# Kernel tuning notes

Measured on AMD Instinct MI355X. Metric: run time of the kernel, lower is better.

Reference implementation:

```python
import jax, jax.numpy as jnp
import numpy as np

T, B, S, H, E, V = 16, 32, 256, 256, 300, 1000


def setup_inputs() -> dict:
    key = jax.random.key(0)
    ks = jax.random.split(key, 16)
    p = lambda k, shp: (jax.random.normal(k, shp, dtype=jnp.float32) * 0.05)
    return {
        "target_variable": jax.random.randint(ks[0], (T, B), 0, V),
        "h0": p(ks[1], (1, B, H)),
        "c0": p(ks[2], (1, B, H)),
        "encoder_outputs": jax.random.normal(ks[3], (S, B, H), dtype=jnp.float32),
        "encoder_lens": jax.random.randint(ks[4], (B,), 1, S + 1),
        "embedding": p(ks[5], (V, E)),
        "W_ih": p(ks[6], (4 * H, E)),
        "W_hh": p(ks[7], (4 * H, H)),
        "b_ih": p(ks[8], (4 * H,)),
        "b_hh": p(ks[9], (4 * H,)),
        "We": p(ks[10], (H, H)),
        "be": p(ks[11], (H,)),
        "Wd": p(ks[12], (H, H)),
        "bd": p(ks[13], (H,)),
        "wa": p(ks[14], (H,)),
        "ba": p(ks[14], (1,)),
        "W_out": p(ks[15], (V, 2 * H)),
        "b_out": p(ks[15], (V,)),
    }


def _lstm(x, h0, c0, W_ih, W_hh, b_ih, b_hh):
    # x: [T,B,E]; torch gate order i,f,g,o
    x_proj = jnp.einsum('tbe,ge->tbg', x, W_ih) + b_ih  # [T,B,4H]
    def step(carry, xg):
        h, c = carry
        g = xg + h @ W_hh.T + b_hh
        i, f, gg, o = jnp.split(g, 4, axis=-1)
        c = jax.nn.sigmoid(f) * c + jax.nn.sigmoid(i) * jnp.tanh(gg)
        h = jax.nn.sigmoid(o) * jnp.tanh(c)
        return (h, c), h
    (hT, cT), outs = jax.lax.scan(step, (h0[0], c0[0]), x_proj)
    return outs, hT[None], cT[None]


def reference(target_variable, h0, c0, encoder_outputs, encoder_lens,
              embedding, W_ih, W_hh, b_ih, b_hh,
              We, be, Wd, bd, wa, ba, W_out, b_out):
    emb = embedding[target_variable]                      # [T,B,E] (dropout p=0 -> identity)
    output, hT, cT = _lstm(emb, h0, c0, W_ih, W_hh, b_ih, b_hh)  # output [T,B,H]
    # additive attention: same math as expand+Linear, applied before broadcast
    enc_t = jnp.einsum('sbh,gh->sbg', encoder_outputs, We) + be   # [S,B,H]
    dec_t = jnp.einsum('tbh,gh->tbg', output, Wd) + bd            # [T,B,H]
    scores = jnp.einsum('tsbh,h->tsb', jnp.tanh(enc_t[None, :, :, :] + dec_t[:, None, :, :]), wa) + ba[0]
    raw_attention = jnp.transpose(scores, (2, 0, 1))              # [B,T,S]
    valid = (jnp.arange(S)[None, None, :] < encoder_lens[:, None, None])  # [B,1,S]
    raw_attention = jnp.where(valid, raw_attention, -jnp.inf)
    attention = jax.nn.softmax(raw_attention, axis=2)             # [B,T,S]
    enc_bf = jnp.transpose(encoder_outputs, (1, 0, 2))            # [B,S,H]
    context = jnp.einsum('bts,bsh->bth', attention, enc_bf)       # [B,T,H]
    out_bf = jnp.transpose(output, (1, 0, 2))                     # [B,T,H]
    combined = jnp.transpose(jnp.concatenate([context, out_bf], axis=2), (1, 0, 2))  # [T,B,2H]
    logits = jnp.einsum('tbh,vh->tbv', combined, W_out) + b_out
    output_prob = jax.nn.softmax(logits, axis=2)                  # [T,B,V]
    return output_prob, hT, cT, context
```

## Files before the change

kernel.cpp:

```cpp
#include <hip/hip_runtime.h>
#include <hip/hip_fp16.h>
#include <math.h>

typedef unsigned int u32;
typedef unsigned short u16;

#define T_ 16
#define B_ 32
#define S_ 256
#define H_ 256
#define E_ 300
#define V_ 1000

typedef _Float16 h2_t __attribute__((ext_vector_type(2)));
typedef __fp16  fp16v2 __attribute__((ext_vector_type(2)));

__device__ __forceinline__ float fast_tanh(float x) {
    return 1.0f - 2.0f / (__expf(2.0f * x) + 1.0f);
}
__device__ __forceinline__ float fast_sigm(float x) {
    return 1.0f / (1.0f + __expf(-x));
}
__device__ __forceinline__ float bf2f(u16 x) { return __uint_as_float(((u32)x) << 16); }
__device__ __forceinline__ float blo(u32 u) { return __uint_as_float(u << 16); }
__device__ __forceinline__ float bhi(u32 u) { return __uint_as_float(u & 0xffff0000u); }
__device__ __forceinline__ u16 f2bf(float f) {
    u32 u = __float_as_uint(f);
    u32 r = (u + 0x7fffu + ((u >> 16) & 1u)) >> 16;
    return (u16)r;
}
__device__ __forceinline__ h2_t u2h2(u32 u) {
    union { u32 a; h2_t b; } c; c.a = u; return c.b;
}
__device__ __forceinline__ u32 pk2(float a, float b) {
    union { fp16v2 v; u32 u; } c; c.v = __builtin_amdgcn_cvt_pkrtz(a, b); return c.u;
}
__device__ __forceinline__ float dot2f16(u32 w, u32 h, float acc) {
#if __has_builtin(__builtin_amdgcn_fdot2)
    return __builtin_amdgcn_fdot2(u2h2(w), u2h2(h), acc, false);
#else
    h2_t wv = u2h2(w), hv = u2h2(h);
    return acc + (float)wv.x * (float)hv.x + (float)wv.y * (float)hv.y;
#endif
}

__device__ void gemm_tile_256(const float* __restrict__ A, const int* __restrict__ gidx,
                              int lda, const float* __restrict__ Bw,
                              const float* __restrict__ bias, float* __restrict__ C,
                              int N, int K, int ldc, int bm, int bn)
{
    __shared__ float As[32][64];
    __shared__ float Bs[32][64];
    const int tid = threadIdx.x;
    const int ty = tid >> 4, tx = tid & 15;
    const int lr = tid >> 2;
    const int lk = (tid & 3) * 8;

    int am = bm + lr;
    int arow = gidx ? gidx[am] : am;
    const float* Ap = A + (size_t)arow * lda;
    int bnr = bn + lr;
    const float* Bp = (bnr < N) ? (Bw + (size_t)bnr * K) : nullptr;

    float acc[4][4] = {};

    for (int k0 = 0; k0 < K; k0 += 32) {
        int kb = k0 + lk;
        float av[8];
        if (kb + 8 <= K) {
            float4 p0 = *(const float4*)(Ap + kb);
            float4 p1 = *(const float4*)(Ap + kb + 4);
            av[0]=p0.x; av[1]=p0.y; av[2]=p0.z; av[3]=p0.w;
            av[4]=p1.x; av[5]=p1.y; av[6]=p1.z; av[7]=p1.w;
        } else {
            #pragma unroll
            for (int j = 0; j < 8; j++) av[j] = (kb + j < K) ? Ap[kb + j] : 0.0f;
        }
        #pragma unroll
        for (int j = 0; j < 8; j++) As[lk + j][lr] = av[j];
        if (Bp && kb + 8 <= K) {
            float4 p0 = *(const float4*)(Bp + kb);
            float4 p1 = *(const float4*)(Bp + kb + 4);
            av[0]=p0.x; av[1]=p0.y; av[2]=p0.z; av[3]=p0.w;
            av[4]=p1.x; av[5]=p1.y; av[6]=p1.z; av[7]=p1.w;
        } else if (Bp) {
            #pragma unroll
            for (int j = 0; j < 8; j++) av[j] = (kb + j < K) ? Bp[kb + j] : 0.0f;
        } else {
            #pragma unroll
            for (int j = 0; j < 8; j++) av[j] = 0.0f;
        }
        #pragma unroll
        for (int j = 0; j < 8; j++) Bs[lk + j][lr] = av[j];
        __syncthreads();
        #pragma unroll
        for (int kk = 0; kk < 32; kk++) {
            float4 a = *(const float4*)&As[kk][ty * 4];
            float4 b = *(const float4*)&Bs[kk][tx * 4];
            acc[0][0] += a.x*b.x; acc[0][1] += a.x*b.y; acc[0][2] += a.x*b.z; acc[0][3] += a.x*b.w;
            acc[1][0] += a.y*b.x; acc[1][1] += a.y*b.y; acc[1][2] += a.y*b.z; acc[1][3] += a.y*b.w;
            acc[2][0] += a.z*b.x; acc[2][1] += a.z*b.y; acc[2][2] += a.z*b.z; acc[2][3] += a.z*b.w;
            acc[3][0] += a.w*b.x; acc[3][1] += a.w*b.y; acc[3][2] += a.w*b.z; acc[3][3] += a.w*b.w;
        }
        __syncthreads();
    }
    #pragma unroll
    for (int i = 0; i < 4; i++) {
        int m = bm + ty * 4 + i;
        #pragma unroll
        for (int j = 0; j < 4; j++) {
            int n = bn + tx * 4 + j;
            if (n < N) C[(size_t)m * ldc + n] = acc[i][j] + bias[n];
        }
    }
}

__global__ __launch_bounds__(256)
void prep_xproj(const float* __restrict__ emb, const int* __restrict__ tv,
                const float* __restrict__ W_ih, const float* __restrict__ b_ih,
                float* __restrict__ xproj,
                const float* __restrict__ Whh,  u32* __restrict__ Wt2,
                const float* __restrict__ Wd,   float* __restrict__ Wdt,
                const float* __restrict__ W_out, u16* __restrict__ WoTb)
{
    const int bid = blockIdx.x;
    if (bid < 128) {
        gemm_tile_256(emb, tv, E_, W_ih, b_ih, xproj, 1024, E_, 1024,
                      (bid >> 4) * 64, (bid & 15) * 64);
        return;
    }
    __shared__ float tile[64][65];
    const int tid = threadIdx.x;
    const int wv = tid >> 6;
    const int lane = tid & 63;

    if (bid < 192) {
        int t = bid - 128;
        int r0 = (t >> 2) * 64, k0 = (t & 3) * 64;
        #pragma unroll 4
        for (int j = 0; j < 16; j++) {
            int row = wv * 16 + j;
            tile[row][lane] = Whh[(size_t)(r0 + row) * 256 + k0 + lane];
        }
        __syncthreads();
        #pragma unroll
        for (int it = 0; it < 2; it++) {
            int q = wv + 4 * it;
            uint4 val;
            val.x = pk2(tile[lane][8*q + 0], tile[lane][8*q + 1]);
            val.y = pk2(tile[lane][8*q + 2], tile[lane][8*q + 3]);
            val.z = pk2(tile[lane][8*q + 4], tile[lane][8*q + 5]);
            val.w = pk2(tile[lane][8*q + 6], tile[lane][8*q + 7]);
            ((uint4*)Wt2)[(size_t)((k0 >> 3) + q) * 1024 + r0 + lane] = val;
        }
    } else if (bid < 208) {
        int t = bid - 192;
        int h0 = (t >> 2) * 64, k0 = (t & 3) * 64;
        #pragma unroll 4
        for (int j = 0; j < 16; j++) {
            int row = wv * 16 + j;
            tile[row][lane] = Wd[(size_t)(h0 + row) * 256 + k0 + lane];
        }
        __syncthreads();
        #pragma unroll
        for (int it = 0; it < 4; it++) {
            int q = wv + 4 * it;
            float4 v;
            v.x = tile[lane][4*q + 0];
            v.y = tile[lane][4*q + 1];
            v.z = tile[lane][4*q + 2];
            v.w = tile[lane][4*q + 3];
            ((float4*)Wdt)[(size_t)((k0 >> 2) + q) * 256 + h0 + lane] = v;
        }
    } else {
        int t = bid - 208;
        int v0 = (t >> 3) * 64, k0 = (t & 7) * 64;
        #pragma unroll 4
        for (int j = 0; j < 16; j++) {
            int row = wv * 16 + j;
            int v = v0 + row;
            tile[row][lane] = (v < V_) ? W_out[(size_t)v * 512 + k0 + lane] : 0.0f;
        }
        __syncthreads();
        #pragma unroll
        for (int it = 0; it < 4; it++) {
            int q = wv + 4 * it;
            int v = v0 + lane;
            float a0 = tile[lane][4*q + 0], a1 = tile[lane][4*q + 1];
            float a2 = tile[lane][4*q + 2], a3 = tile[lane][4*q + 3];
            float b0 = __shfl_xor(a0, 1, 64), b1 = __shfl_xor(a1, 1, 64);
            float b2 = __shfl_xor(a2, 1, 64), b3 = __shfl_xor(a3, 1, 64);
            if (!(lane & 1) && v < V_) {
                uint4 w;
                w.x = (u32)f2bf(a0) | ((u32)f2bf(b0) << 16);
                w.y = (u32)f2bf(a1) | ((u32)f2bf(b1) << 16);
                w.z = (u32)f2bf(a2) | ((u32)f2bf(b2) << 16);
                w.w = (u32)f2bf(a3) | ((u32)f2bf(b3) << 16);
                ((uint4*)WoTb)[(size_t)((k0 >> 2) + q) * 500 + (v >> 1)] = w;
            }
        }
    }
}

__global__ __launch_bounds__(1024, 4)
void lstm_enct(const float* __restrict__ xproj,
               const u32*   __restrict__ Wt2,
               const float* __restrict__ bhh,
               const float* __restrict__ h0, const float* __restrict__ c0,
               float* __restrict__ combined,
               float* __restrict__ hT, float* __restrict__ cT,
               const float* __restrict__ enc_raw,
               const float* __restrict__ We,
               const float* __restrict__ be,
               float* __restrict__ enct)
{
    const int bid = blockIdx.x;
    const int tid = threadIdx.x;
    __shared__ float zs[1024], cs[256];
    __shared__ u32 hp[128];
    __shared__ float As2[32][132];
    __shared__ float Bs2[32][132];

    if (bid < 32) {
        const int b = bid;
        const int r = tid;
        if (tid < 256) {
            float h0v = h0[b * 256 + tid];
            cs[tid] = c0[b * 256 + tid];
            float hpart = __shfl_xor(h0v, 1, 64);
            if (!(tid & 1)) hp[tid >> 1] = pk2(h0v, hpart);
        }
        const float bh = bhh[r];
        const uint4* wp4 = (const uint4*)Wt2 + r;
        __syncthreads();

        for (int t = 0; t < T_; t++) {
            float xp = xproj[((size_t)t * B_ + b) * 1024 + r];
            float acc = 0.0f;
            const uint4* hp4 = (const uint4*)hp;
            #pragma unroll 8
            for (int i = 0; i < 32; i++) {
                uint4 hv = hp4[i];
                uint4 w  = wp4[(size_t)i * 1024];
                acc = dot2f16(w.x, hv.x, acc);
                acc = dot2f16(w.y, hv.y, acc);
                acc = dot2f16(w.z, hv.z, acc);
                acc = dot2f16(w.w, hv.w, acc);
            }
            zs[r] = xp + bh + acc;
            __syncthreads();

            if (tid < 256) {
                float ig = fast_sigm(zs[tid]);
                float fg = fast_sigm(zs[256 + tid]);
                float gg = fast_tanh(zs[512 + tid]);
                float og = fast_sigm(zs[768 + tid]);
                float c = fg * cs[tid] + ig * gg;
                float h = og * fast_tanh(c);
                cs[tid] = c;
                combined[((size_t)t * B_ + b) * 512 + 256 + tid] = h;
                if (t == T_ - 1) {
                    hT[b * 256 + tid] = h;
                    cT[b * 256 + tid] = c;
                }
                float hpart = __shfl_xor(h, 1, 64);
                if (!(tid & 1)) hp[tid >> 1] = pk2(h, hpart);
            }
            __syncthreads();
        }
    } else {
        const int tile = bid - 32;
        const int bm = (tile >> 1) * 128;
        const int bn = (tile & 1) * 128;
        const int tx = tid & 31, ty = tid >> 5;
        const int lr = tid >> 3;
        const int lk = (tid & 7) * 4;

        const float* Ap = enc_raw + (size_t)(bm + lr) * 256;
        const float* Bp = We + (size_t)(bn + lr) * 256;
        float acc[4][4] = {};

        for (int k0 = 0; k0 < 256; k0 += 32) {
            float4 a4 = *(const float4*)(Ap + k0 + lk);
            float4 b4 = *(const float4*)(Bp + k0 + lk);
            As2[lk + 0][lr] = a4.x; As2[lk + 1][lr] = a4.y;
            As2[lk + 2][lr] = a4.z; As2[lk + 3][lr] = a4.w;
            Bs2[lk + 0][lr] = b4.x; Bs2[lk + 1][lr] = b4.y;
            Bs2[lk + 2][lr] = b4.z; Bs2[lk + 3][lr] = b4.w;
            __syncthreads();
            #pragma unroll
            for (int kk = 0; kk < 32; kk++) {
                float4 a = *(const float4*)&As2[kk][ty * 4];
                float4 b = *(const float4*)&Bs2[kk][tx * 4];
                acc[0][0] += a.x*b.x; acc[0][1] += a.x*b.y; acc[0][2] += a.x*b.z; acc[0][3] += a.x*b.w;
                acc[1][0] += a.y*b.x; acc[1][1] += a.y*b.y; acc[1][2] += a.y*b.z; acc[1][3] += a.y*b.w;
                acc[2][0] += a.z*b.x; acc[2][1] += a.z*b.y; acc[2][2] += a.z*b.z; acc[2][3] += a.z*b.w;
                acc[3][0] += a.w*b.x; acc[3][1] += a.w*b.y; acc[3][2] += a.w*b.z; acc[3][3] += a.w*b.w;
            }
            __syncthreads();
        }
        #pragma unroll
        for (int i = 0; i < 4; i++) {
            int m = bm + ty * 4 + i;
            #pragma unroll
            for (int j = 0; j < 4; j++) {
                int n = bn + tx * 4 + j;
                enct[(size_t)m * 256 + n] = acc[i][j] + be[n];
            }
        }
    }
}

__global__ __launch_bounds__(512)
void attn_logits(const float* __restrict__ enct,
                 const float* __restrict__ combined_in,
                 const float* __restrict__ Wdt,
                 const float* __restrict__ bd,
                 const float* __restrict__ enc_raw,
                 const float* __restrict__ wa, const float* __restrict__ ba,
                 const int* __restrict__ lens,
                 const u16* __restrict__ WoTb,
                 const float* __restrict__ b_out,
                 float* __restrict__ ctx_out,
                 float* __restrict__ probs)
{
    const int bid = blockIdx.x;
    const int b = bid & 31;
    const int t = bid >> 5;
    const int tid = threadIdx.x;
    const int wv = tid >> 6, lane = tid & 63;
    __shared__ float ds[256], was[256], sc[256];
    __shared__ float crow[512];
    __shared__ float tmp2[512];
    __shared__ float lrow[1000];
    __shared__ float red[8], red2[8];

    if (tid < 256) {
        crow[256 + tid] = combined_in[((size_t)t * B_ + b) * 512 + 256 + tid];
        was[tid] = wa[tid];
    }
    const int len = lens[b];
    const float bav = ba[0];
    __syncthreads();

    {
        const int h   = tid & 255;
        const int kq0 = (tid >> 8) * 32;
        float acc = 0.0f;
        const float4* wp = (const float4*)Wdt + h;
        #pragma unroll 8
        for (int kq = kq0; kq < kq0 + 32; kq++) {
            float4 w = wp[(size_t)kq * 256];
            float4 c = *(const float4*)&crow[256 + kq * 4];
            acc += w.x * c.x;
            acc += w.y * c.y;
            acc += w.z * c.z;
            acc += w.w * c.w;
        }
        tmp2[tid] = acc;
    }
    __syncthreads();
    if (tid < 256) ds[tid] = bd[tid] + tmp2[tid] + tmp2[tid + 256];
    __syncthreads();

    for (int s = wv; s < len; s += 8) {
        const float* er = enct + ((size_t)s * B_ + b) * 256;
        float sum = 0.0f;
        #pragma unroll
        for (int j = 0; j < 4; j++) {
            int h = lane + 64 * j;
            sum += fast_tanh(er[h] + ds[h]) * was[h];
        }
        #pragma unroll
        for (int off = 32; off >= 1; off >>= 1) sum += __shfl_xor(sum, off, 64);
        if (lane == 0) sc[s] = sum + bav;
    }
    __syncthreads();

    float x = (tid < len) ? sc[tid] : -INFINITY;
    float m = x;
    #pragma unroll
    for (int off = 32; off >= 1; off >>= 1) m = fmaxf(m, __shfl_xor(m, off, 64));
    if (lane == 0) red[wv] = m;
    __syncthreads();
    m = red[0];
    #pragma unroll
    for (int i = 1; i < 8; i++) m = fmaxf(m, red[i]);
    float e = __expf(x - m);
    float ssum = e;
    #pragma unroll
    for (int off = 32; off >= 1; off >>= 1) ssum += __shfl_xor(ssum, off, 64);
    if (lane == 0) red2[wv] = ssum;
    __syncthreads();
    ssum = red2[0] + red2[1] + red2[2] + red2[3] + red2[4] + red2[5] + red2[6] + red2[7];
    if (tid < 256) sc[tid] = e / ssum;
    __syncthreads();

    {
        const int h  = tid & 255;
        const int sg = tid >> 8;
        const int mid = (len + 1) >> 1;
        const int s0 = sg ? mid : 0;
        const int s1 = sg ? len : mid;
        float cacc = 0.0f;
        const float* eb = enc_raw + (size_t)b * 256 + h;
        #pragma unroll 4
        for (int s = s0; s < s1; s++) cacc += sc[s] * eb[(size_t)s * (B_ * H_)];
        tmp2[tid] = cacc;
    }
    __syncthreads();
    if (tid < 256) {
        float ctx = tmp2[tid] + tmp2[tid + 256];
        ctx_out[((size_t)b * T_ + t) * 256 + tid] = ctx;
        crow[tid] = ctx;
    }
    __syncthreads();

    if (tid < 500) {
        const int v0 = tid * 2;
        float a0 = b_out[v0], a1 = b_out[v0 + 1];
        const uint4* wp = (const uint4*)WoTb + tid;
        #pragma unroll 8
        for (int kq = 0; kq < 128; kq++) {
            uint4 w = wp[(size_t)kq * 500];
            float4 c = *(const float4*)&crow[kq * 4];
            a0 += c.x * blo(w.x); a1 += c.x * bhi(w.x);
            a0 += c.y * blo(w.y); a1 += c.y * bhi(w.y);
            a0 += c.z * blo(w.z); a1 += c.z * bhi(w.z);
            a0 += c.w * blo(w.w); a1 += c.w * bhi(w.w);
        }
        lrow[v0] = a0;
        lrow[v0 + 1] = a1;
    }
    __syncthreads();

    float v0v = -INFINITY, v1v = -INFINITY;
    if (tid < 500) { v0v = lrow[tid * 2]; v1v = lrow[tid * 2 + 1]; }
    float mx = fmaxf(v0v, v1v);
    #pragma unroll
    for (int off = 32; off >= 1; off >>= 1) mx = fmaxf(mx, __shfl_xor(mx, off, 64));
    if (lane == 0) red[wv] = mx;
    __syncthreads();
    mx = red[0];
    #pragma unroll
    for (int i = 1; i < 8; i++) mx = fmaxf(mx, red[i]);
    float e0 = __expf(v0v - mx), e1 = __expf(v1v - mx);
    float s2 = e0 + e1;
    #pragma unroll
    for (int off = 32; off >= 1; off >>= 1) s2 += __shfl_xor(s2, off, 64);
    if (lane == 0) red2[wv] = s2;
    __syncthreads();
    s2 = red2[0] + red2[1] + red2[2] + red2[3] + red2[4] + red2[5] + red2[6] + red2[7];
    float inv = 1.0f / s2;
    if (tid < 500) {
        float2 pv = make_float2(e0 * inv, e1 * inv);
        *(float2*)&probs[((size_t)t * B_ + b) * V_ + tid * 2] = pv;
    }
}

extern "C" void kernel_launch(void* const* d_in, const int* in_sizes, int n_in,
                              void* d_out, int out_size, void* d_ws, size_t ws_size,
                              hipStream_t stream) {
    const int*   tv       = (const int*)d_in[0];
    const float* h0       = (const float*)d_in[1];
    const float* c0       = (const float*)d_in[2];
    const float* enc_raw  = (const float*)d_in[3];
    const int*   lens     = (const int*)d_in[4];
    const float* emb      = (const float*)d_in[5];
    const float* W_ih     = (const float*)d_in[6];
    const float* W_hh     = (const float*)d_in[7];
    const float* b_ih     = (const float*)d_in[8];
    const float* b_hh     = (const float*)d_in[9];
    const float* We       = (const float*)d_in[10];
    const float* be       = (const float*)d_in[11];
    const float* Wd       = (const float*)d_in[12];
    const float* bd       = (const float*)d_in[13];
    const float* wa       = (const float*)d_in[14];
    const float* ba       = (const float*)d_in[15];
    const float* W_out    = (const float*)d_in[16];
    const float* b_out    = (const float*)d_in[17];

    float* ws       = (float*)d_ws;
    float* enct     = ws;
    float* xproj    = ws + 2097152;
    float* Wdt      = ws + 2621440;
    u16*   WoTb     = (u16*)(ws + 2752512);
    float* combined = ws + 3264512;
    u32*   Wt2      = (u32*)(ws + 3526656);

    float* out      = (float*)d_out;
    float* probs    = out;
    float* hT       = out + 512000;
    float* cT       = out + 520192;
    float* ctx_out  = out + 528384;

    prep_xproj<<<336, 256, 0, stream>>>(emb, tv, W_ih, b_ih, xproj,
                                        W_hh, Wt2, Wd, Wdt, W_out, WoTb);
    lstm_enct<<<160, 1024, 0, stream>>>(xproj, Wt2, b_hh, h0, c0, combined, hT, cT,
                                        enc_raw, We, be, enct);
    attn_logits<<<512, 512, 0, stream>>>(enct, combined, Wdt, bd, enc_raw,
                                         wa, ba, lens, WoTb, b_out, ctx_out, probs);
}
```

Before: 240.5 us.

## Keep LSTM recurrent weights resident in registers and LDS across timesteps

In the LSTM recurrence branch, half of each thread's W_hh slice (16 uint4) is loaded into registers once and a quarter is staged into LDS once. Only the remaining quarter is still streamed from global memory on each of the 16 timesteps. This is meant to cut the repeated global/L2 weight traffic on the sequential critical path. In exchange it uses a large shared buffer (~134KB, aliased with the GEMM tiles) and 64 extra VGPRs per thread at 1024 threads per block, which may exceed the register budget and spill or cut occupancy for the GEMM blocks that share the kernel.

```diff
diff --git a/kernel.cpp b/kernel.cpp
--- a/kernel.cpp
+++ b/kernel.cpp
@@ -216,12 +216,13 @@
 {
     const int bid = blockIdx.x;
     const int tid = threadIdx.x;
-    __shared__ float zs[1024], cs[256];
-    __shared__ u32 hp[128];
-    __shared__ float As2[32][132];
-    __shared__ float Bs2[32][132];
+    __shared__ __align__(16) u32 smem[34176];
 
     if (bid < 32) {
+        float* zs = (float*)smem;
+        float* cs = (float*)(smem + 1024);
+        u32*   hp = smem + 1280;
+        u32*   wlds = smem + 1408;
         const int b = bid;
         const int r = tid;
         if (tid < 256) {
@@ -232,20 +233,52 @@
         }
         const float bh = bhh[r];
         const uint4* wp4 = (const uint4*)Wt2 + r;
+
+        uint4 wreg[16];
+        #pragma unroll
+        for (int j = 0; j < 16; j++) wreg[j] = wp4[(size_t)(16 + j) * 1024];
+        #pragma unroll
+        for (int j = 0; j < 8; j++) {
+            uint4 w = wp4[(size_t)(8 + j) * 1024];
+            wlds[(j * 4 + 0) * 1024 + r] = w.x;
+            wlds[(j * 4 + 1) * 1024 + r] = w.y;
+            wlds[(j * 4 + 2) * 1024 + r] = w.z;
+            wlds[(j * 4 + 3) * 1024 + r] = w.w;
+        }
         __syncthreads();
 
         for (int t = 0; t < T_; t++) {
             float xp = xproj[((size_t)t * B_ + b) * 1024 + r];
             float acc = 0.0f;
             const uint4* hp4 = (const uint4*)hp;
-            #pragma unroll 8
-            for (int i = 0; i < 32; i++) {
+            #pragma unroll
+            for (int i = 0; i < 8; i++) {
                 uint4 hv = hp4[i];
                 uint4 w  = wp4[(size_t)i * 1024];
                 acc = dot2f16(w.x, hv.x, acc);
                 acc = dot2f16(w.y, hv.y, acc);
                 acc = dot2f16(w.z, hv.z, acc);
                 acc = dot2f16(w.w, hv.w, acc);
+            }
+            #pragma unroll
+            for (int j = 0; j < 8; j++) {
+                uint4 hv = hp4[8 + j];
+                u32 w0 = wlds[(j * 4 + 0) * 1024 + r];
+                u32 w1 = wlds[(j * 4 + 1) * 1024 + r];
+                u32 w2 = wlds[(j * 4 + 2) * 1024 + r];
+                u32 w3 = wlds[(j * 4 + 3) * 1024 + r];
+                acc = dot2f16(w0, hv.x, acc);
+                acc = dot2f16(w1, hv.y, acc);
+                acc = dot2f16(w2, hv.z, acc);
+                acc = dot2f16(w3, hv.w, acc);
+            }
+            #pragma unroll
+            for (int j = 0; j < 16; j++) {
+                uint4 hv = hp4[16 + j];
+                acc = dot2f16(wreg[j].x, hv.x, acc);
+                acc = dot2f16(wreg[j].y, hv.y, acc);
+                acc = dot2f16(wreg[j].z, hv.z, acc);
+                acc = dot2f16(wreg[j].w, hv.w, acc);
             }
             zs[r] = xp + bh + acc;
             __syncthreads();
@@ -269,6 +302,8 @@
             __syncthreads();
         }
     } else {
+        float (*As2)[132] = (float (*)[132])smem;
+        float (*Bs2)[132] = (float (*)[132])(smem + 4224);
         const int tile = bid - 32;
         const int bm = (tile >> 1) * 128;
         const int bn = (tile & 1) * 128;
```

Result: faster. 213.3 us (-11.3%).
